# Optimization experiments

Measured on AMD Instinct MI355X. Metric: run time of the kernel, lower is better.

Reference implementation:

```python
import jax, jax.numpy as jnp
import numpy as np

WIDTH = 64  # attention_width

def setup_inputs() -> dict:
    key = jax.random.key(0)
    ks = jax.random.split(key, 4)
    B, T, D, U = 4, 1024, 1024, 64
    x = jax.random.normal(ks[0], (B, T, D), dtype=jnp.float32)
    Wt = jax.random.normal(ks[1], (D, U), dtype=jnp.float32) * (1.0 / np.sqrt(D))
    Wx = jax.random.normal(ks[2], (D, U), dtype=jnp.float32) * (1.0 / np.sqrt(D))
    bh = jnp.zeros((U,), dtype=jnp.float32)
    Wa = jax.random.normal(ks[3], (U, 1), dtype=jnp.float32) * (1.0 / np.sqrt(U))
    ba = jnp.zeros((1,), dtype=jnp.float32)
    return {"x": x, "Wt": Wt, "Wx": Wx, "bh": bh, "Wa": Wa, "ba": ba}


def reference(x, Wt, Wx, bh, Wa, ba):
    B, T, D = x.shape
    # additive emission: h = tanh(q_i + k_j + bh), e_ij = h @ Wa + ba
    q = jnp.einsum('btd,du->btu', x, Wt)  # [B,T,U]
    k = jnp.einsum('btd,du->btu', x, Wx)  # [B,T,U]
    h = jnp.tanh(q[:, :, None, :] + k[:, None, :, :] + bh)  # [B,T,T,U]
    e = jnp.einsum('btsu,uo->bts', h, Wa) + ba[0]  # [B,T,T]
    # local-width band mask (width centered, history_only=False)
    idx = jnp.arange(T)
    lower = (idx - WIDTH // 2)[:, None]           # [T,1]
    upper = lower + WIDTH
    band = (lower <= idx[None, :]) & (idx[None, :] < upper)  # [T,T]
    e = e - 10000.0 * (1.0 - band.astype(e.dtype))
    a = jax.nn.softmax(e, axis=-1)  # [B,T,T]
    v = jnp.einsum('bts,bsd->btd', a, x)
    return v
```

## Files before the change

### kernel.cpp

```cpp
#include <hip/hip_runtime.h>

#define BB 4
#define TT 1024
#define DD 1024
#define UU 64
#define HW 32

typedef unsigned short u16;
typedef __attribute__((ext_vector_type(4))) unsigned short u16x4;
typedef __attribute__((ext_vector_type(8))) unsigned short u16x8;
typedef __attribute__((ext_vector_type(8))) short bf16x8;
typedef __attribute__((ext_vector_type(4))) float f32x4;
typedef __attribute__((ext_vector_type(2))) float f32x2;

__device__ __forceinline__ u16 bf16_rne(float f) {
  unsigned b = __builtin_bit_cast(unsigned, f);
  b += 0x7FFFu + ((b >> 16) & 1u);
  return (u16)(b >> 16);
}
__device__ __forceinline__ float bf16_tof(u16 h) {
  return __builtin_bit_cast(float, ((unsigned)h) << 16);
}

#define WLD 65
__global__ __launch_bounds__(256) void wprep_kernel(
    const float* __restrict__ Wt, const float* __restrict__ Wx,
    u16* __restrict__ Wht, u16* __restrict__ Wlt)
{
  __shared__ float ws[128 * WLD];
  const int tid = threadIdx.x;
  const int d0  = blockIdx.x * 128;
  const float* __restrict__ src = blockIdx.y ? Wx : Wt;

  for (int i = tid; i < 2048; i += 256) {
    int r  = i >> 4;
    int c4 = (i & 15) << 2;
    float4 v = *(const float4*)(src + (size_t)(d0 + r) * UU + c4);
    float* w = ws + r * WLD + c4;
    w[0] = v.x; w[1] = v.y; w[2] = v.z; w[3] = v.w;
  }
  __syncthreads();

  for (int it = tid; it < 1024; it += 256) {
    int u = it >> 4, oct = it & 15;
    u16x8 h, l;
    #pragma unroll
    for (int j = 0; j < 8; ++j) {
      float v = ws[(8 * oct + j) * WLD + u];
      u16 hh = bf16_rne(v);
      h[j] = hh;
      l[j] = bf16_rne(v - bf16_tof(hh));
    }
    size_t off = (size_t)(blockIdx.y * UU + u) * DD + d0 + 8 * oct;
    *(u16x8*)(Wht + off) = h;
    *(u16x8*)(Wlt + off) = l;
  }
}

#define PROWS 16
#define XLD (DD + 8)

__global__ __launch_bounds__(512) void proj_mfma_kernel(
    const float* __restrict__ x, const u16* __restrict__ Wht,
    const u16* __restrict__ Wlt, const float* __restrict__ bh,
    float* __restrict__ qo, float* __restrict__ ko)
{
  __shared__ __align__(16) u16 Xh[PROWS][XLD];
  __shared__ __align__(16) u16 Xl[PROWS][XLD];

  const int tid  = threadIdx.x;
  const int row0 = blockIdx.x * PROWS;

  {
    const float4* src = (const float4*)(x + (size_t)row0 * DD);
    #pragma unroll
    for (int i = 0; i < 8; ++i) {
      int idx4 = tid + 512 * i;
      int r    = idx4 >> 8;
      int k4   = (idx4 & 255) << 2;
      float4 v = src[idx4];
      float vv[4] = {v.x, v.y, v.z, v.w};
      u16x4 hv, lv;
      #pragma unroll
      for (int j = 0; j < 4; ++j) {
        u16 hh = bf16_rne(vv[j]);
        float lf = vv[j] - bf16_tof(hh);
        hv[j] = hh;
        lv[j] = bf16_rne(lf);
      }
      *(u16x4*)&Xh[r][k4] = hv;
      *(u16x4*)&Xl[r][k4] = lv;
    }
  }
  __syncthreads();

  const int lane = tid & 63;
  const int wv   = tid >> 6;
  const int arow = lane & 15;
  const int g    = lane >> 4;
  const int u0   = wv * 16;

  const u16* ah_p = &Xh[arow][8 * g];
  const u16* al_p = &Xl[arow][8 * g];
  const u16* bh_p = Wht + (size_t)(u0 + arow) * DD + 8 * g;
  const u16* bl_p = Wlt + (size_t)(u0 + arow) * DD + 8 * g;

  f32x4 acc0 = {0.f, 0.f, 0.f, 0.f};
  f32x4 acc1 = {0.f, 0.f, 0.f, 0.f};
  f32x4 acc2 = {0.f, 0.f, 0.f, 0.f};
  f32x4 acc3 = {0.f, 0.f, 0.f, 0.f};

  #pragma unroll 8
  for (int ks = 0; ks < 32; ++ks) {
    bf16x8 ah = *(const bf16x8*)(ah_p + 32 * ks);
    bf16x8 al = *(const bf16x8*)(al_p + 32 * ks);
    bf16x8 bhv = *(const bf16x8*)(bh_p + 32 * ks);
    bf16x8 blv = *(const bf16x8*)(bl_p + 32 * ks);
    acc0 = __builtin_amdgcn_mfma_f32_16x16x32_bf16(ah, bhv, acc0, 0, 0, 0);
    acc1 = __builtin_amdgcn_mfma_f32_16x16x32_bf16(ah, blv, acc1, 0, 0, 0);
    acc2 = __builtin_amdgcn_mfma_f32_16x16x32_bf16(al, bhv, acc2, 0, 0, 0);
    acc3 = __builtin_amdgcn_mfma_f32_16x16x32_bf16(al, blv, acc3, 0, 0, 0);
  }

  const int col  = u0 + arow;
  const float bias = (col < UU) ? bh[col] : 0.0f;
  float* dst = (col < UU) ? (qo + col) : (ko + (col - UU));
  #pragma unroll
  for (int r = 0; r < 4; ++r) {
    float v = acc0[r] + acc1[r] + acc2[r] + acc3[r];
    dst[(size_t)(row0 + 4 * g + r) * UU] = __expf(-2.0f * (v + bias));
  }
}

__global__ __launch_bounds__(512) void band_kernel(
    const float* __restrict__ x,  const float* __restrict__ eqg,
    const float* __restrict__ ekg, const float* __restrict__ Wa,
    const float* __restrict__ ba, float* __restrict__ out)
{
  __shared__ __align__(16) float at[72 * 8];

  const int tid  = threadIdx.x;
  const int bid  = blockIdx.x;
  const int tile = (bid & 7) * 64 + (bid >> 3);
  const int b    = tile >> 7;
  const int i0   = (tile & 127) * 8;

  const int jlo = max(0, i0 - HW);
  const int jhi = min(TT, i0 + 8 - 1 + HW);
  const int NJ  = jhi - jlo;

  const float bav = ba[0];

  {
    const int w    = tid >> 6;
    const int lane = tid & 63;
    const int g    = lane >> 3;
    const int uc   = (lane & 7) * 8;
    float eqv[8], wv[8];
    {
      const float* qp = eqg + (size_t)(b * TT + i0 + g) * UU + uc;
      float4 a0 = *(const float4*)qp;
      float4 a1 = *(const float4*)(qp + 4);
      eqv[0] = a0.x; eqv[1] = a0.y; eqv[2] = a0.z; eqv[3] = a0.w;
      eqv[4] = a1.x; eqv[5] = a1.y; eqv[6] = a1.z; eqv[7] = a1.w;
      float4 wa0 = *(const float4*)(Wa + uc);
      float4 wa1 = *(const float4*)(Wa + uc + 4);
      wv[0] = wa0.x; wv[1] = wa0.y; wv[2] = wa0.z; wv[3] = wa0.w;
      wv[4] = wa1.x; wv[5] = wa1.y; wv[6] = wa1.z; wv[7] = wa1.w;
    }
    const int ig = i0 + g;
    const float* kbase = ekg + (size_t)(b * TT + jlo) * UU + uc;
    for (int j = w; j < NJ; j += 8) {
      const float* kp = kbase + (size_t)j * UU;
      float4 k0 = *(const float4*)kp;
      float4 k1 = *(const float4*)(kp + 4);
      float ekv[8] = {k0.x, k0.y, k0.z, k0.w, k1.x, k1.y, k1.z, k1.w};
      float s0 = 0.f;
      #pragma unroll
      for (int s = 0; s < 8; ++s) {
        float t  = eqv[s] * ekv[s];
        float th = (1.0f - t) * __builtin_amdgcn_rcpf(1.0f + t);
        s0 = __builtin_fmaf(th, wv[s], s0);
      }
      s0 += __shfl_xor(s0, 1);
      s0 += __shfl_xor(s0, 2);
      s0 += __shfl_xor(s0, 4);
      const int jg = jlo + j;
      const bool inband = (jg >= ig - HW) && (jg < ig + HW);
      if ((lane & 7) == 0) at[j * 8 + g] = inband ? (s0 + bav) : -1e30f;
    }
  }
  __syncthreads();

  {
    const int row = tid >> 6;
    const int l   = tid & 63;
    float v0 = (l      < NJ) ? at[(l     ) * 8 + row] : -1e30f;
    float v1 = (l + 64 < NJ) ? at[(l + 64) * 8 + row] : -1e30f;
    float m = fmaxf(v0, v1);
    #pragma unroll
    for (int off = 32; off >= 1; off >>= 1) m = fmaxf(m, __shfl_xor(m, off));
    float e0 = __expf(v0 - m);
    float e1 = __expf(v1 - m);
    float ssum = e0 + e1;
    #pragma unroll
    for (int off = 32; off >= 1; off >>= 1) ssum += __shfl_xor(ssum, off);
    float inv = 1.0f / ssum;
    if (l      < NJ) at[(l     ) * 8 + row] = e0 * inv;
    if (l + 64 < NJ) at[(l + 64) * 8 + row] = e1 * inv;
  }
  __syncthreads();

  {
    const f32x2 z = {0.f, 0.f};
    f32x2 vacc[8];
    #pragma unroll
    for (int i = 0; i < 8; ++i) vacc[i] = z;
    const float* xb = x + (size_t)(b * TT + jlo) * DD + 2 * tid;
    #pragma unroll 4
    for (int j = 0; j < NJ; ++j) {
      f32x2 xv = *(const f32x2*)(xb + (size_t)j * DD);
      float4 a0 = *(const float4*)(at + j * 8);
      float4 a1 = *(const float4*)(at + j * 8 + 4);
      float av[8] = {a0.x, a0.y, a0.z, a0.w, a1.x, a1.y, a1.z, a1.w};
      #pragma unroll
      for (int i = 0; i < 8; ++i) {
        f32x2 s = {av[i], av[i]};
        vacc[i] = s * xv + vacc[i];
      }
    }
    float* ob = out + (size_t)(b * TT + i0) * DD + 2 * tid;
    #pragma unroll
    for (int i = 0; i < 8; ++i) *(f32x2*)(ob + (size_t)i * DD) = vacc[i];
  }
}

extern "C" void kernel_launch(void* const* d_in, const int* in_sizes, int n_in,
                              void* d_out, int out_size, void* d_ws, size_t ws_size,
                              hipStream_t stream) {
  const float* x  = (const float*)d_in[0];
  const float* Wt = (const float*)d_in[1];
  const float* Wx = (const float*)d_in[2];
  const float* bh = (const float*)d_in[3];
  const float* Wa = (const float*)d_in[4];
  const float* ba = (const float*)d_in[5];
  float* out = (float*)d_out;

  float* q = (float*)d_ws;
  float* k = q + (size_t)BB * TT * UU;
  u16* Wht = (u16*)(k + (size_t)BB * TT * UU);
  u16* Wlt = Wht + (size_t)128 * DD;

  wprep_kernel<<<dim3(8, 2), dim3(256), 0, stream>>>(Wt, Wx, Wht, Wlt);
  proj_mfma_kernel<<<dim3((BB * TT) / PROWS), dim3(512), 0, stream>>>(x, Wht, Wlt, bh, q, k);
  band_kernel<<<dim3((BB * TT) / 8), dim3(512), 0, stream>>>(x, q, k, Wa, ba, out);
}
```

Baseline: 115.8 us.

## Double rows per block in projection and band kernels for weight/x reuse

The projection kernel now handles 32 rows per block instead of 16, staging x in two K-halves so shared memory stays small, and reuses each loaded weight fragment across two MFMA row tiles. The band kernel processes 16 query rows per block instead of 8, so each loaded key vector and each x row in the weighted sum serve twice as many queries. This halves redundant global traffic for W and for the overlapping x halo, at the cost of more registers, an extra barrier per phase, and half as many blocks (less parallelism).

```diff
diff --git a/kernel.cpp b/kernel.cpp
--- a/kernel.cpp
+++ b/kernel.cpp
@@ -57,42 +57,20 @@
   }
 }
 
-#define PROWS 16
-#define XLD (DD + 8)
-
-__global__ __launch_bounds__(512) void proj_mfma_kernel(
+#define PROWS 32
+#define KH 512
+#define KXLD (KH + 8)
+
+__global__ __launch_bounds__(512, 4) void proj_mfma_kernel(
     const float* __restrict__ x, const u16* __restrict__ Wht,
     const u16* __restrict__ Wlt, const float* __restrict__ bh,
     float* __restrict__ qo, float* __restrict__ ko)
 {
-  __shared__ __align__(16) u16 Xh[PROWS][XLD];
-  __shared__ __align__(16) u16 Xl[PROWS][XLD];
+  __shared__ __align__(16) u16 Xh[PROWS][KXLD];
+  __shared__ __align__(16) u16 Xl[PROWS][KXLD];
 
   const int tid  = threadIdx.x;
   const int row0 = blockIdx.x * PROWS;
-
-  {
-    const float4* src = (const float4*)(x + (size_t)row0 * DD);
-    #pragma unroll
-    for (int i = 0; i < 8; ++i) {
-      int idx4 = tid + 512 * i;
-      int r    = idx4 >> 8;
-      int k4   = (idx4 & 255) << 2;
-      float4 v = src[idx4];
-      float vv[4] = {v.x, v.y, v.z, v.w};
-      u16x4 hv, lv;
-      #pragma unroll
-      for (int j = 0; j < 4; ++j) {
-        u16 hh = bf16_rne(vv[j]);
-        float lf = vv[j] - bf16_tof(hh);
-        hv[j] = hh;
-        lv[j] = bf16_rne(lf);
-      }
-      *(u16x4*)&Xh[r][k4] = hv;
-      *(u16x4*)&Xl[r][k4] = lv;
-    }
-  }
-  __syncthreads();
 
   const int lane = tid & 63;
   const int wv   = tid >> 6;
@@ -100,26 +78,57 @@
   const int g    = lane >> 4;
   const int u0   = wv * 16;
 
-  const u16* ah_p = &Xh[arow][8 * g];
-  const u16* al_p = &Xl[arow][8 * g];
-  const u16* bh_p = Wht + (size_t)(u0 + arow) * DD + 8 * g;
-  const u16* bl_p = Wlt + (size_t)(u0 + arow) * DD + 8 * g;
-
-  f32x4 acc0 = {0.f, 0.f, 0.f, 0.f};
-  f32x4 acc1 = {0.f, 0.f, 0.f, 0.f};
-  f32x4 acc2 = {0.f, 0.f, 0.f, 0.f};
-  f32x4 acc3 = {0.f, 0.f, 0.f, 0.f};
-
-  #pragma unroll 8
-  for (int ks = 0; ks < 32; ++ks) {
-    bf16x8 ah = *(const bf16x8*)(ah_p + 32 * ks);
-    bf16x8 al = *(const bf16x8*)(al_p + 32 * ks);
-    bf16x8 bhv = *(const bf16x8*)(bh_p + 32 * ks);
-    bf16x8 blv = *(const bf16x8*)(bl_p + 32 * ks);
-    acc0 = __builtin_amdgcn_mfma_f32_16x16x32_bf16(ah, bhv, acc0, 0, 0, 0);
-    acc1 = __builtin_amdgcn_mfma_f32_16x16x32_bf16(ah, blv, acc1, 0, 0, 0);
-    acc2 = __builtin_amdgcn_mfma_f32_16x16x32_bf16(al, bhv, acc2, 0, 0, 0);
-    acc3 = __builtin_amdgcn_mfma_f32_16x16x32_bf16(al, blv, acc3, 0, 0, 0);
+  f32x4 a00 = {0,0,0,0}, a01 = {0,0,0,0}, a02 = {0,0,0,0}, a03 = {0,0,0,0};
+  f32x4 a10 = {0,0,0,0}, a11 = {0,0,0,0}, a12 = {0,0,0,0}, a13 = {0,0,0,0};
+
+  #pragma unroll
+  for (int ph = 0; ph < 2; ++ph) {
+    const int kb = ph * KH;
+    if (ph) __syncthreads();
+
+    #pragma unroll
+    for (int i = 0; i < 8; ++i) {
+      int idx4 = tid + 512 * i;
+      int r    = idx4 >> 7;
+      int c4   = (idx4 & 127) << 2;
+      float4 v = *(const float4*)(x + (size_t)(row0 + r) * DD + kb + c4);
+      float vv[4] = {v.x, v.y, v.z, v.w};
+      u16x4 hv, lv;
+      #pragma unroll
+      for (int j = 0; j < 4; ++j) {
+        u16 hh = bf16_rne(vv[j]);
+        hv[j] = hh;
+        lv[j] = bf16_rne(vv[j] - bf16_tof(hh));
+      }
+      *(u16x4*)&Xh[r][c4] = hv;
+      *(u16x4*)&Xl[r][c4] = lv;
+    }
+    __syncthreads();
+
+    const u16* bhp = Wht + (size_t)(u0 + arow) * DD + kb + 8 * g;
+    const u16* blp = Wlt + (size_t)(u0 + arow) * DD + kb + 8 * g;
+    const u16* xh0 = &Xh[arow][8 * g];
+    const u16* xl0 = &Xl[arow][8 * g];
+    const u16* xh1 = &Xh[arow + 16][8 * g];
+    const u16* xl1 = &Xl[arow + 16][8 * g];
+
+    #pragma unroll 4
+    for (int ks = 0; ks < 16; ++ks) {
+      bf16x8 bhv = *(const bf16x8*)(bhp + 32 * ks);
+      bf16x8 blv = *(const bf16x8*)(blp + 32 * ks);
+      bf16x8 ah0 = *(const bf16x8*)(xh0 + 32 * ks);
+      bf16x8 al0 = *(const bf16x8*)(xl0 + 32 * ks);
+      bf16x8 ah1 = *(const bf16x8*)(xh1 + 32 * ks);
+      bf16x8 al1 = *(const bf16x8*)(xl1 + 32 * ks);
+      a00 = __builtin_amdgcn_mfma_f32_16x16x32_bf16(ah0, bhv, a00, 0, 0, 0);
+      a01 = __builtin_amdgcn_mfma_f32_16x16x32_bf16(ah0, blv, a01, 0, 0, 0);
+      a02 = __builtin_amdgcn_mfma_f32_16x16x32_bf16(al0, bhv, a02, 0, 0, 0);
+      a03 = __builtin_amdgcn_mfma_f32_16x16x32_bf16(al0, blv, a03, 0, 0, 0);
+      a10 = __builtin_amdgcn_mfma_f32_16x16x32_bf16(ah1, bhv, a10, 0, 0, 0);
+      a11 = __builtin_amdgcn_mfma_f32_16x16x32_bf16(ah1, blv, a11, 0, 0, 0);
+      a12 = __builtin_amdgcn_mfma_f32_16x16x32_bf16(al1, bhv, a12, 0, 0, 0);
+      a13 = __builtin_amdgcn_mfma_f32_16x16x32_bf16(al1, blv, a13, 0, 0, 0);
+    }
   }
 
   const int col  = u0 + arow;
@@ -127,26 +136,29 @@
   float* dst = (col < UU) ? (qo + col) : (ko + (col - UU));
   #pragma unroll
   for (int r = 0; r < 4; ++r) {
-    float v = acc0[r] + acc1[r] + acc2[r] + acc3[r];
-    dst[(size_t)(row0 + 4 * g + r) * UU] = __expf(-2.0f * (v + bias));
-  }
-}
-
+    float v0 = a00[r] + a01[r] + a02[r] + a03[r];
+    float v1 = a10[r] + a11[r] + a12[r] + a13[r];
+    dst[(size_t)(row0 +      4 * g + r) * UU] = __expf(-2.0f * (v0 + bias));
+    dst[(size_t)(row0 + 16 + 4 * g + r) * UU] = __expf(-2.0f * (v1 + bias));
+  }
+}
+
+#define QBLK 16
 __global__ __launch_bounds__(512) void band_kernel(
     const float* __restrict__ x,  const float* __restrict__ eqg,
     const float* __restrict__ ekg, const float* __restrict__ Wa,
     const float* __restrict__ ba, float* __restrict__ out)
 {
-  __shared__ __align__(16) float at[72 * 8];
+  __shared__ __align__(16) float at[80 * 16];
 
   const int tid  = threadIdx.x;
   const int bid  = blockIdx.x;
-  const int tile = (bid & 7) * 64 + (bid >> 3);
-  const int b    = tile >> 7;
-  const int i0   = (tile & 127) * 8;
+  const int tile = (bid & 7) * 32 + (bid >> 3);
+  const int b    = tile >> 6;
+  const int i0   = (tile & 63) * QBLK;
 
   const int jlo = max(0, i0 - HW);
-  const int jhi = min(TT, i0 + 8 - 1 + HW);
+  const int jhi = min(TT, i0 + QBLK - 1 + HW);
   const int NJ  = jhi - jlo;
 
   const float bav = ba[0];
@@ -156,82 +168,98 @@
     const int lane = tid & 63;
     const int g    = lane >> 3;
     const int uc   = (lane & 7) * 8;
-    float eqv[8], wv[8];
+    float eq0[8], eq1[8], wv[8];
     {
-      const float* qp = eqg + (size_t)(b * TT + i0 + g) * UU + uc;
-      float4 a0 = *(const float4*)qp;
-      float4 a1 = *(const float4*)(qp + 4);
-      eqv[0] = a0.x; eqv[1] = a0.y; eqv[2] = a0.z; eqv[3] = a0.w;
-      eqv[4] = a1.x; eqv[5] = a1.y; eqv[6] = a1.z; eqv[7] = a1.w;
+      const float* q0 = eqg + (size_t)(b * TT + i0 + g) * UU + uc;
+      const float* q1 = q0 + 8 * UU;
+      float4 c0 = *(const float4*)q0,      c1 = *(const float4*)(q0 + 4);
+      float4 d0 = *(const float4*)q1,      d1 = *(const float4*)(q1 + 4);
+      eq0[0]=c0.x; eq0[1]=c0.y; eq0[2]=c0.z; eq0[3]=c0.w;
+      eq0[4]=c1.x; eq0[5]=c1.y; eq0[6]=c1.z; eq0[7]=c1.w;
+      eq1[0]=d0.x; eq1[1]=d0.y; eq1[2]=d0.z; eq1[3]=d0.w;
+      eq1[4]=d1.x; eq1[5]=d1.y; eq1[6]=d1.z; eq1[7]=d1.w;
       float4 wa0 = *(const float4*)(Wa + uc);
       float4 wa1 = *(const float4*)(Wa + uc + 4);
-      wv[0] = wa0.x; wv[1] = wa0.y; wv[2] = wa0.z; wv[3] = wa0.w;
-      wv[4] = wa1.x; wv[5] = wa1.y; wv[6] = wa1.z; wv[7] = wa1.w;
-    }
-    const int ig = i0 + g;
+      wv[0]=wa0.x; wv[1]=wa0.y; wv[2]=wa0.z; wv[3]=wa0.w;
+      wv[4]=wa1.x; wv[5]=wa1.y; wv[6]=wa1.z; wv[7]=wa1.w;
+    }
+    const int ig0 = i0 + g;
+    const int ig1 = i0 + 8 + g;
     const float* kbase = ekg + (size_t)(b * TT + jlo) * UU + uc;
     for (int j = w; j < NJ; j += 8) {
       const float* kp = kbase + (size_t)j * UU;
       float4 k0 = *(const float4*)kp;
       float4 k1 = *(const float4*)(kp + 4);
       float ekv[8] = {k0.x, k0.y, k0.z, k0.w, k1.x, k1.y, k1.z, k1.w};
-      float s0 = 0.f;
+      float s0 = 0.f, s1 = 0.f;
       #pragma unroll
       for (int s = 0; s < 8; ++s) {
-        float t  = eqv[s] * ekv[s];
-        float th = (1.0f - t) * __builtin_amdgcn_rcpf(1.0f + t);
-        s0 = __builtin_fmaf(th, wv[s], s0);
-      }
-      s0 += __shfl_xor(s0, 1);
-      s0 += __shfl_xor(s0, 2);
-      s0 += __shfl_xor(s0, 4);
+        float t0  = eq0[s] * ekv[s];
+        float t1  = eq1[s] * ekv[s];
+        float th0 = (1.0f - t0) * __builtin_amdgcn_rcpf(1.0f + t0);
+        float th1 = (1.0f - t1) * __builtin_amdgcn_rcpf(1.0f + t1);
+        s0 = __builtin_fmaf(th0, wv[s], s0);
+        s1 = __builtin_fmaf(th1, wv[s], s1);
+      }
+      s0 += __shfl_xor(s0, 1); s1 += __shfl_xor(s1, 1);
+      s0 += __shfl_xor(s0, 2); s1 += __shfl_xor(s1, 2);
+      s0 += __shfl_xor(s0, 4); s1 += __shfl_xor(s1, 4);
       const int jg = jlo + j;
-      const bool inband = (jg >= ig - HW) && (jg < ig + HW);
-      if ((lane & 7) == 0) at[j * 8 + g] = inband ? (s0 + bav) : -1e30f;
+      if ((lane & 7) == 0) {
+        at[j * 16 + g]     = (jg >= ig0 - HW && jg < ig0 + HW) ? (s0 + bav) : -1e30f;
+        at[j * 16 + 8 + g] = (jg >= ig1 - HW && jg < ig1 + HW) ? (s1 + bav) : -1e30f;
+      }
     }
   }
   __syncthreads();
 
   {
-    const int row = tid >> 6;
-    const int l   = tid & 63;
-    float v0 = (l      < NJ) ? at[(l     ) * 8 + row] : -1e30f;
-    float v1 = (l + 64 < NJ) ? at[(l + 64) * 8 + row] : -1e30f;
-    float m = fmaxf(v0, v1);
-    #pragma unroll
-    for (int off = 32; off >= 1; off >>= 1) m = fmaxf(m, __shfl_xor(m, off));
-    float e0 = __expf(v0 - m);
-    float e1 = __expf(v1 - m);
-    float ssum = e0 + e1;
-    #pragma unroll
-    for (int off = 32; off >= 1; off >>= 1) ssum += __shfl_xor(ssum, off);
-    float inv = 1.0f / ssum;
-    if (l      < NJ) at[(l     ) * 8 + row] = e0 * inv;
-    if (l + 64 < NJ) at[(l + 64) * 8 + row] = e1 * inv;
+    const int w = tid >> 6;
+    const int l = tid & 63;
+    #pragma unroll
+    for (int rr2 = 0; rr2 < 2; ++rr2) {
+      const int rr = 2 * w + rr2;
+      float v0 = (l      < NJ) ? at[(l     ) * 16 + rr] : -1e30f;
+      float v1 = (l + 64 < NJ) ? at[(l + 64) * 16 + rr] : -1e30f;
+      float m = fmaxf(v0, v1);
+      #pragma unroll
+      for (int off = 32; off >= 1; off >>= 1) m = fmaxf(m, __shfl_xor(m, off));
+      float e0 = __expf(v0 - m);
+      float e1 = __expf(v1 - m);
+      float ssum = e0 + e1;
+      #pragma unroll
+      for (int off = 32; off >= 1; off >>= 1) ssum += __shfl_xor(ssum, off);
+      float inv = 1.0f / ssum;
+      if (l      < NJ) at[(l     ) * 16 + rr] = e0 * inv;
+      if (l + 64 < NJ) at[(l + 64) * 16 + rr] = e1 * inv;
+    }
   }
   __syncthreads();
 
   {
     const f32x2 z = {0.f, 0.f};
-    f32x2 vacc[8];
-    #pragma unroll
-    for (int i = 0; i < 8; ++i) vacc[i] = z;
+    f32x2 vacc[16];
+    #pragma unroll
+    for (int i = 0; i < 16; ++i) vacc[i] = z;
     const float* xb = x + (size_t)(b * TT + jlo) * DD + 2 * tid;
-    #pragma unroll 4
+    #pragma unroll 2
     for (int j = 0; j < NJ; ++j) {
       f32x2 xv = *(const f32x2*)(xb + (size_t)j * DD);
-      float4 a0 = *(const float4*)(at + j * 8);
-      float4 a1 = *(const float4*)(at + j * 8 + 4);
-      float av[8] = {a0.x, a0.y, a0.z, a0.w, a1.x, a1.y, a1.z, a1.w};
-      #pragma unroll
-      for (int i = 0; i < 8; ++i) {
+      float4 a0 = *(const float4*)(at + j * 16);
+      float4 a1 = *(const float4*)(at + j * 16 + 4);
+      float4 a2 = *(const float4*)(at + j * 16 + 8);
+      float4 a3 = *(const float4*)(at + j * 16 + 12);
+      float av[16] = {a0.x, a0.y, a0.z, a0.w, a1.x, a1.y, a1.z, a1.w,
+                      a2.x, a2.y, a2.z, a2.w, a3.x, a3.y, a3.z, a3.w};
+      #pragma unroll
+      for (int i = 0; i < 16; ++i) {
         f32x2 s = {av[i], av[i]};
         vacc[i] = s * xv + vacc[i];
       }
     }
     float* ob = out + (size_t)(b * TT + i0) * DD + 2 * tid;
     #pragma unroll
-    for (int i = 0; i < 8; ++i) *(f32x2*)(ob + (size_t)i * DD) = vacc[i];
+    for (int i = 0; i < 16; ++i) *(f32x2*)(ob + (size_t)i * DD) = vacc[i];
   }
 }
 
@@ -253,5 +281,5 @@
 
   wprep_kernel<<<dim3(8, 2), dim3(256), 0, stream>>>(Wt, Wx, Wht, Wlt);
   proj_mfma_kernel<<<dim3((BB * TT) / PROWS), dim3(512), 0, stream>>>(x, Wht, Wlt, bh, q, k);
-  band_kernel<<<dim3((BB * TT) / 8), dim3(512), 0, stream>>>(x, q, k, Wa, ba, out);
-}
+  band_kernel<<<dim3((BB * TT) / QBLK), dim3(512), 0, stream>>>(x, q, k, Wa, ba, out);
+}
```

After: 123.6 us. 1.07x slower.
